# Kernel optimization log

Hardware: AMD Instinct MI355X
Metric: run time of the kernel (lower is better)

The kernel has to match this reference:

```python
import jax, jax.numpy as jnp
import numpy as np

B, Cin, Cout, K, H, W = 16, 32, 32, 3, 256, 256
EMB = 256  # layer_pos_embedding_size == condition_size == 256


def setup_inputs() -> dict:
    key = jax.random.key(0)
    ks = jax.random.split(key, 7)
    return {
        "x": jax.random.normal(ks[0], (B, Cin, H, W), jnp.float32),
        "condition": jax.random.normal(ks[1], (B, EMB), jnp.float32),
        "layer_pos_embedding": jax.random.normal(ks[2], (B, EMB), jnp.float32),
        # base conv weight, stored [Cin, Cout, K, K] as in the torch module
        "weights": jax.random.normal(ks[3], (Cin, Cout, K, K), jnp.float32) * 0.05,
        "bias": jax.random.normal(ks[4], (Cout,), jnp.float32) * 0.05,
        # weightAdapt: Linear(2*EMB -> Cin); biasAdapt: Linear(2*EMB -> Cout)
        "wa_w": jax.random.normal(ks[5], (Cin, 2 * EMB), jnp.float32) * 0.04,
        "wa_b": jnp.zeros((Cin,), jnp.float32),
        "ba_w": jax.random.normal(ks[6], (Cout, 2 * EMB), jnp.float32) * 0.04,
        "ba_b": jnp.zeros((Cout,), jnp.float32),
    }


def reference(x, condition, layer_pos_embedding, weights, bias, wa_w, wa_b, ba_w, ba_b):
    # i = cat([condition, layer_pos_embedding])  -> [B, 2*EMB]
    i = jnp.concatenate([condition, layer_pos_embedding], axis=-1)
    wadapt = i @ wa_w.T + wa_b   # [B, Cin]  per-sample input-channel modulation
    badapt = i @ ba_w.T + ba_b   # [B, Cout] per-sample bias modulation
    # per-sample OIHW kernel: (weights [Cin,Cout,K,K] * wadapt[b,Cin,1,1,1]) rearranged
    kern = jnp.einsum('iokl,bi->boikl', weights, wadapt)  # [B, Cout, Cin, K, K]

    def conv1(xi, ki):
        # xi: [Cin,H,W], ki: [Cout,Cin,K,K] -> [Cout,H,W], padding='same', stride 1
        return jax.lax.conv_general_dilated(
            xi[None], ki, window_strides=(1, 1), padding='SAME',
            dimension_numbers=('NCHW', 'OIHW', 'NCHW'))[0]

    o = jax.vmap(conv1)(x, kern)  # [B, Cout, H, W] (== groups=batch grouped conv)
    # modulated bias add per (batch, out_channel)
    return o + (bias[None, :] * badapt)[:, :, None, None]
```

## Files before the change

kernel.cpp:

```cpp
#include <hip/hip_runtime.h>


#define B_    16
#define CIN   32
#define COUT  32
#define H_    256
#define W_    256
#define EMB2  512

#define XPX       66
#define PXS       32
#define ROWS_     (XPX*PXS)
#define NSLOT     8

using short8  = __attribute__((ext_vector_type(8))) short;
using float4v = __attribute__((ext_vector_type(4))) float;

__device__ __forceinline__ unsigned short f2bf(float f) {
    unsigned u = __builtin_bit_cast(unsigned, f);
    u += 0x7FFFu + ((u >> 16) & 1u);
    return (unsigned short)(u >> 16);
}
__device__ __forceinline__ unsigned pk2(float a, float b) {
    return (unsigned)f2bf(a) | ((unsigned)f2bf(b) << 16);
}

__global__ __launch_bounds__(256) void adapt_kernel(
    const float* __restrict__ cond, const float* __restrict__ lpe,
    const float* __restrict__ wa_w, const float* __restrict__ wa_b,
    const float* __restrict__ ba_w, const float* __restrict__ ba_b,
    const float* __restrict__ bias, float* __restrict__ ws)
{
    __shared__ float iv[EMB2];
    __shared__ float partial[64][4];
    const int b = blockIdx.x;
    const int t = threadIdx.x;

    iv[t]       = cond[b*256 + t];
    iv[t + 256] = lpe[b*256 + t];
    __syncthreads();

    const int out  = t & 63;
    const int part = t >> 6;
    const float* row = (out < 32) ? (wa_w + out*EMB2) : (ba_w + (out-32)*EMB2);
    float s = 0.f;
    #pragma unroll 8
    for (int j = part*128; j < part*128 + 128; ++j) s += iv[j] * row[j];
    partial[out][part] = s;
    __syncthreads();

    if (t < 64) {
        float v = partial[t][0] + partial[t][1] + partial[t][2] + partial[t][3];
        if (t < 32) ws[b*32 + t] = v + wa_b[t];
        else {
            int o = t - 32;
            ws[512 + b*32 + o] = bias[o] * (v + ba_b[o]);
        }
    }
}

__global__ __launch_bounds__(256, 2) void conv_kernel(
    const float* __restrict__ x, const float* __restrict__ weights,
    const float* __restrict__ ws, float* __restrict__ out)
{
    __shared__ unsigned short xbuf[NSLOT * ROWS_];
    __shared__ unsigned short wbuf[9 * COUT * PXS];

    const int tid    = threadIdx.x;
    const int lane   = tid & 63;
    const int w      = tid >> 6;
    const int ln15   = lane & 15;
    const int kg     = lane >> 4;
    const int xstrip = blockIdx.x * 64;
    const int ystrip = blockIdx.y * 32;
    const int b      = blockIdx.z;

    for (int idx = tid; idx < CIN*COUT*9; idx += 256) {
        int i   = idx / 288;
        int rem = idx - i*288;
        int o   = rem / 9;
        int tap = rem - o*9;
        float v = weights[idx] * ws[b*32 + i];
        wbuf[tap*1024 + o*32 + i] = f2bf(v);
    }

    auto stage = [&](int r0, int nrows) {
        const int total = nrows * XPX * 4;
        for (int idx = tid; idx < total; idx += 256) {
            int p  = idx % XPX;
            int t2 = idx / XPX;
            int g  = t2 & 3;
            int rr = t2 >> 2;
            int r  = r0 + rr;
            int gy = ystrip + r;
            int gx = xstrip + p - 1;
            int slot = (r + 1) & 7;
            unsigned dst = slot*ROWS_ + p*PXS + ((g ^ ((p >> 1) & 3)) * 8);
            uint4 pk;
            if (((unsigned)gy < 256u) & ((unsigned)gx < 256u)) {
                const float* src = x + (((size_t)(b*CIN + g*8) << 16) + (gy << 8) + gx);
                float f0 = src[0*65536], f1 = src[1*65536];
                float f2 = src[2*65536], f3 = src[3*65536];
                float f4 = src[4*65536], f5 = src[5*65536];
                float f6 = src[6*65536], f7 = src[7*65536];
                pk.x = pk2(f0, f1); pk.y = pk2(f2, f3);
                pk.z = pk2(f4, f5); pk.w = pk2(f6, f7);
            } else {
                pk = uint4{0u, 0u, 0u, 0u};
            }
            *(uint4*)&xbuf[dst] = pk;
        }
    };

    stage(-1, 6);
    __syncthreads();

    short8 wA[9][2];
    #pragma unroll
    for (int tap = 0; tap < 9; ++tap)
        #pragma unroll
        for (int ot = 0; ot < 2; ++ot) {
            int o = ot*16 + ln15;
            wA[tap][ot] = *(const short8*)&wbuf[tap*1024 + o*32 + kg*8];
        }

    float bm[2][4];
    #pragma unroll
    for (int ot = 0; ot < 2; ++ot)
        #pragma unroll
        for (int r = 0; r < 4; ++r)
            bm[ot][r] = ws[512 + b*32 + ot*16 + kg*4 + r];

    for (int t = 0; t < 8; ++t) {
        if (t > 0) {
            stage(4*t + 1, 4);
            __syncthreads();
        }

        const int orow = 4*t + w;
        const int gy   = ystrip + orow;

        float4v acc[4][2];
        #pragma unroll
        for (int c = 0; c < 4; ++c) {
            acc[c][0] = float4v{0.f, 0.f, 0.f, 0.f};
            acc[c][1] = float4v{0.f, 0.f, 0.f, 0.f};
        }

        #pragma unroll
        for (int dy = 0; dy < 3; ++dy) {
            const int rowbase = ((orow + dy) & 7) * ROWS_;
            #pragma unroll
            for (int dx = 0; dx < 3; ++dx) {
                const int tap = dy*3 + dx;
                #pragma unroll
                for (int c = 0; c < 4; ++c) {
                    int p = c*16 + dx + ln15;
                    int a = rowbase + p*PXS + ((kg ^ ((p >> 1) & 3)) * 8);
                    short8 xf = *(const short8*)&xbuf[a];
                    acc[c][0] = __builtin_amdgcn_mfma_f32_16x16x32_bf16(
                                    wA[tap][0], xf, acc[c][0], 0, 0, 0);
                    acc[c][1] = __builtin_amdgcn_mfma_f32_16x16x32_bf16(
                                    wA[tap][1], xf, acc[c][1], 0, 0, 0);
                }
            }
        }
        __syncthreads();

        #pragma unroll
        for (int c = 0; c < 4; ++c) {
            const int xcol = xstrip + c*16 + ln15;
            #pragma unroll
            for (int ot = 0; ot < 2; ++ot) {
                const int obase = ot*16 + kg*4;
                #pragma unroll
                for (int r = 0; r < 4; ++r) {
                    out[(((size_t)(b*COUT + obase + r) << 8) + gy << 8) + xcol] =
                        acc[c][ot][r] + bm[ot][r];
                }
            }
        }
    }
}

extern "C" void kernel_launch(void* const* d_in, const int* in_sizes, int n_in,
                              void* d_out, int out_size, void* d_ws, size_t ws_size,
                              hipStream_t stream) {
    const float* x       = (const float*)d_in[0];
    const float* cond    = (const float*)d_in[1];
    const float* lpe     = (const float*)d_in[2];
    const float* weights = (const float*)d_in[3];
    const float* bias    = (const float*)d_in[4];
    const float* wa_w    = (const float*)d_in[5];
    const float* wa_b    = (const float*)d_in[6];
    const float* ba_w    = (const float*)d_in[7];
    const float* ba_b    = (const float*)d_in[8];
    float* outp = (float*)d_out;
    float* ws   = (float*)d_ws;

    adapt_kernel<<<dim3(B_), dim3(256), 0, stream>>>(
        cond, lpe, wa_w, wa_b, ba_w, ba_b, bias, ws);

    conv_kernel<<<dim3(W_/64, H_/32, B_), dim3(256), 0, stream>>>(
        x, weights, ws, outp);
}
```

Measured before the change: 277.9 us.

## Software-pipeline input row staging via register prefetch overlapping MFMA compute

The conv kernel now issues global loads for the next four input rows into registers before running the MFMA loop, then packs them into shared memory after the compute and stores, so load latency overlaps compute. The weight buffer now aliases the input ring buffer, which cuts LDS use, and launch bounds rise to 3 blocks per CU for more occupancy. The adapt kernel is rewritten to use wave shuffles instead of shared-memory reductions. The risk is higher register pressure from 40 prefetch floats per thread alongside the weight fragments and accumulators, which may cause spills under the tighter 3-block bound.

```diff
diff --git a/kernel.cpp b/kernel.cpp
--- a/kernel.cpp
+++ b/kernel.cpp
@@ -10,7 +10,7 @@
 
 #define XPX       66
 #define PXS       32
-#define ROWS_     (XPX*PXS)
+#define ROWSZ     (XPX*PXS)
 #define NSLOT     8
 
 using short8  = __attribute__((ext_vector_type(8))) short;
@@ -31,40 +31,41 @@
     const float* __restrict__ ba_w, const float* __restrict__ ba_b,
     const float* __restrict__ bias, float* __restrict__ ws)
 {
-    __shared__ float iv[EMB2];
-    __shared__ float partial[64][4];
-    const int b = blockIdx.x;
-    const int t = threadIdx.x;
-
-    iv[t]       = cond[b*256 + t];
-    iv[t + 256] = lpe[b*256 + t];
-    __syncthreads();
-
-    const int out  = t & 63;
-    const int part = t >> 6;
-    const float* row = (out < 32) ? (wa_w + out*EMB2) : (ba_w + (out-32)*EMB2);
-    float s = 0.f;
-    #pragma unroll 8
-    for (int j = part*128; j < part*128 + 128; ++j) s += iv[j] * row[j];
-    partial[out][part] = s;
-    __syncthreads();
-
-    if (t < 64) {
-        float v = partial[t][0] + partial[t][1] + partial[t][2] + partial[t][3];
-        if (t < 32) ws[b*32 + t] = v + wa_b[t];
-        else {
-            int o = t - 32;
-            ws[512 + b*32 + o] = bias[o] * (v + ba_b[o]);
-        }
-    }
-}
-
-__global__ __launch_bounds__(256, 2) void conv_kernel(
+    const int b    = blockIdx.x;
+    const int lane = threadIdx.x & 63;
+    const int w    = threadIdx.x >> 6;
+
+    float ivr[8];
+    #pragma unroll
+    for (int j = 0; j < 8; ++j) {
+        int e = lane*8 + j;
+        ivr[j] = (e < 256) ? cond[b*256 + e] : lpe[b*256 + e - 256];
+    }
+
+    for (int r = w; r < 64; r += 4) {
+        const float* row = (r < 32) ? (wa_w + r*EMB2) : (ba_w + (r-32)*EMB2);
+        float s = 0.f;
+        #pragma unroll
+        for (int j = 0; j < 8; ++j) s += ivr[j] * row[lane*8 + j];
+        #pragma unroll
+        for (int off = 32; off; off >>= 1) s += __shfl_xor(s, off, 64);
+        if (lane == 0) {
+            if (r < 32) ws[b*32 + r] = s + wa_b[r];
+            else {
+                int o = r - 32;
+                ws[512 + b*32 + o] = bias[o] * (s + ba_b[o]);
+            }
+        }
+    }
+}
+
+__global__ __launch_bounds__(256, 3) void conv_kernel(
     const float* __restrict__ x, const float* __restrict__ weights,
     const float* __restrict__ ws, float* __restrict__ out)
 {
-    __shared__ unsigned short xbuf[NSLOT * ROWS_];
-    __shared__ unsigned short wbuf[9 * COUT * PXS];
+    __shared__ unsigned short smem[NSLOT * ROWSZ];
+    unsigned short* wbuf = smem;
+    unsigned short* xbuf = smem;
 
     const int tid    = threadIdx.x;
     const int lane   = tid & 63;
@@ -80,49 +81,16 @@
         int rem = idx - i*288;
         int o   = rem / 9;
         int tap = rem - o*9;
-        float v = weights[idx] * ws[b*32 + i];
-        wbuf[tap*1024 + o*32 + i] = f2bf(v);
-    }
-
-    auto stage = [&](int r0, int nrows) {
-        const int total = nrows * XPX * 4;
-        for (int idx = tid; idx < total; idx += 256) {
-            int p  = idx % XPX;
-            int t2 = idx / XPX;
-            int g  = t2 & 3;
-            int rr = t2 >> 2;
-            int r  = r0 + rr;
-            int gy = ystrip + r;
-            int gx = xstrip + p - 1;
-            int slot = (r + 1) & 7;
-            unsigned dst = slot*ROWS_ + p*PXS + ((g ^ ((p >> 1) & 3)) * 8);
-            uint4 pk;
-            if (((unsigned)gy < 256u) & ((unsigned)gx < 256u)) {
-                const float* src = x + (((size_t)(b*CIN + g*8) << 16) + (gy << 8) + gx);
-                float f0 = src[0*65536], f1 = src[1*65536];
-                float f2 = src[2*65536], f3 = src[3*65536];
-                float f4 = src[4*65536], f5 = src[5*65536];
-                float f6 = src[6*65536], f7 = src[7*65536];
-                pk.x = pk2(f0, f1); pk.y = pk2(f2, f3);
-                pk.z = pk2(f4, f5); pk.w = pk2(f6, f7);
-            } else {
-                pk = uint4{0u, 0u, 0u, 0u};
-            }
-            *(uint4*)&xbuf[dst] = pk;
-        }
-    };
-
-    stage(-1, 6);
+        wbuf[tap*1024 + o*32 + i] = f2bf(weights[idx] * ws[b*32 + i]);
+    }
     __syncthreads();
 
     short8 wA[9][2];
     #pragma unroll
     for (int tap = 0; tap < 9; ++tap)
         #pragma unroll
-        for (int ot = 0; ot < 2; ++ot) {
-            int o = ot*16 + ln15;
-            wA[tap][ot] = *(const short8*)&wbuf[tap*1024 + o*32 + kg*8];
-        }
+        for (int ot = 0; ot < 2; ++ot)
+            wA[tap][ot] = *(const short8*)&wbuf[tap*1024 + (ot*16 + ln15)*32 + kg*8];
 
     float bm[2][4];
     #pragma unroll
@@ -130,11 +98,65 @@
         #pragma unroll
         for (int r = 0; r < 4; ++r)
             bm[ot][r] = ws[512 + b*32 + ot*16 + kg*4 + r];
+    __syncthreads();
+
+    auto issue_item = [&](int idx, int r0, float* pf) {
+        int p  = idx % XPX;
+        int t2 = idx / XPX;
+        int g  = t2 & 3;
+        int rr = t2 >> 2;
+        int gy = ystrip + r0 + rr;
+        int gx = xstrip + p - 1;
+        int gyc = min(max(gy, 0), 255);
+        int gxc = min(max(gx, 0), 255);
+        const float* src = x + (((size_t)(b*CIN + g*8)) << 16) + (gyc << 8) + gxc;
+        #pragma unroll
+        for (int q = 0; q < 8; ++q) pf[q] = src[(size_t)q << 16];
+    };
+    auto pack_item = [&](int idx, int r0, const float* pf) {
+        int p  = idx % XPX;
+        int t2 = idx / XPX;
+        int g  = t2 & 3;
+        int rr = t2 >> 2;
+        int gy = ystrip + r0 + rr;
+        int gx = xstrip + p - 1;
+        bool ok = ((unsigned)gy < 256u) & ((unsigned)gx < 256u);
+        int slot = (r0 + rr + 1) & 7;
+        unsigned dst = slot*ROWSZ + p*PXS + ((g ^ ((p >> 1) & 3)) * 8);
+        uint4 v;
+        if (ok) {
+            v.x = pk2(pf[0], pf[1]); v.y = pk2(pf[2], pf[3]);
+            v.z = pk2(pf[4], pf[5]); v.w = pk2(pf[6], pf[7]);
+        } else v = uint4{0u,0u,0u,0u};
+        *(uint4*)&xbuf[dst] = v;
+    };
+
+    #pragma unroll
+    for (int hb = 0; hb < 2; ++hb) {
+        const int r0 = -1 + hb*3;
+        float pf[4][8];
+        #pragma unroll
+        for (int it = 0; it < 4; ++it) {
+            int idx = tid + it*256;
+            if (idx < 3*XPX*4) issue_item(idx, r0, pf[it]);
+        }
+        #pragma unroll
+        for (int it = 0; it < 4; ++it) {
+            int idx = tid + it*256;
+            if (idx < 3*XPX*4) pack_item(idx, r0, pf[it]);
+        }
+    }
+    __syncthreads();
 
     for (int t = 0; t < 8; ++t) {
-        if (t > 0) {
-            stage(4*t + 1, 4);
-            __syncthreads();
+        float pf[5][8];
+        const int pr0 = 4*t + 5;
+        if (t < 7) {
+            #pragma unroll
+            for (int it = 0; it < 5; ++it) {
+                int idx = tid + it*256;
+                if (idx < 4*XPX*4) issue_item(idx, pr0, pf[it]);
+            }
         }
 
         const int orow = 4*t + w;
@@ -143,13 +165,13 @@
         float4v acc[4][2];
         #pragma unroll
         for (int c = 0; c < 4; ++c) {
-            acc[c][0] = float4v{0.f, 0.f, 0.f, 0.f};
-            acc[c][1] = float4v{0.f, 0.f, 0.f, 0.f};
+            acc[c][0] = float4v{0.f,0.f,0.f,0.f};
+            acc[c][1] = float4v{0.f,0.f,0.f,0.f};
         }
 
         #pragma unroll
         for (int dy = 0; dy < 3; ++dy) {
-            const int rowbase = ((orow + dy) & 7) * ROWS_;
+            const int rowbase = ((orow + dy) & 7) * ROWSZ;
             #pragma unroll
             for (int dx = 0; dx < 3; ++dx) {
                 const int tap = dy*3 + dx;
@@ -165,7 +187,6 @@
                 }
             }
         }
-        __syncthreads();
 
         #pragma unroll
         for (int c = 0; c < 4; ++c) {
@@ -175,10 +196,20 @@
                 const int obase = ot*16 + kg*4;
                 #pragma unroll
                 for (int r = 0; r < 4; ++r) {
-                    out[(((size_t)(b*COUT + obase + r) << 8) + gy << 8) + xcol] =
-                        acc[c][ot][r] + bm[ot][r];
+                    out[(((size_t)(b*COUT + obase + r) << 8) | (unsigned)gy) * 256
+                        + xcol] = acc[c][ot][r] + bm[ot][r];
                 }
             }
+        }
+
+        if (t < 7) {
+            __syncthreads();
+            #pragma unroll
+            for (int it = 0; it < 5; ++it) {
+                int idx = tid + it*256;
+                if (idx < 4*XPX*4) pack_item(idx, pr0, pf[it]);
+            }
+            __syncthreads();
         }
     }
 }
```

New measurement: 468.6 us. +68.6%, slower.
